# Kernel tuning notes

Hardware: AMD Instinct MI355X
Metric: run time of the kernel (lower is better)

## Reference

```python
import jax, jax.numpy as jnp
import numpy as np

ALPHA = 0.01  # ELU slope from init kwargs


def setup_inputs() -> dict:
    key = jax.random.key(0)
    k1, k2, k3, k4, k5 = jax.random.split(key, 5)
    B, L, D_IN, D_ATT = 8, 2048, 256, 128
    context = jax.random.normal(k1, (B, L, D_IN), dtype=jnp.float32)
    query = jax.random.normal(k2, (B, L, D_IN), dtype=jnp.float32)
    query_mask = jax.random.randint(k3, (B, L), 0, 2, dtype=jnp.int32)
    # Linear(in_size, attention_size, bias=False) weights (stored as [in, out])
    W_in = jax.random.normal(k4, (D_IN, D_ATT), dtype=jnp.float32) * 0.05
    W_mem = jax.random.normal(k5, (D_IN, D_ATT), dtype=jnp.float32) * 0.05
    return {"context": context, "query": query, "W_in": W_in,
            "W_mem": W_mem, "query_mask": query_mask}


def reference(context, query, W_in, W_mem, query_mask):
    # VariationalDropout is identity at inference; Linear -> ELU(alpha=0.01)
    inp = jax.nn.elu(jnp.einsum('bld,df->blf', context, W_in), ALPHA)   # [B, Lc, Datt]
    mem = jax.nn.elu(jnp.einsum('bld,df->blf', query, W_mem), ALPHA)    # [B, Lq, Datt]
    scale = inp.shape[-1] ** 0.5
    logits = jnp.einsum('bcf,bqf->bcq', inp, mem) / scale               # [B, Lc, Lq]
    big = jnp.finfo(logits.dtype).max
    # mask_diag=True: kill diagonal (self) positions
    Lq = logits.shape[-1]
    eye = jnp.eye(Lq, dtype=bool)
    logits = jnp.where(eye[None, :, :], -big, logits)
    # masked_softmax over the query axis using query_mask [B, Lq]
    valid = (query_mask > 0)[:, None, :]                                # [B, 1, Lq]
    logits = jnp.where(valid, logits, -big)
    score = jax.nn.softmax(logits, axis=-1)                             # [B, Lc, Lq]
    return jnp.einsum('bcq,bqd->bcd', score, query)                     # [B, Lc, D_in]
```

## Files before the change

### kernel.cpp

```cpp
#include <hip/hip_runtime.h>
#include <math.h>

typedef short v4s __attribute__((ext_vector_type(4)));
typedef short v8s __attribute__((ext_vector_type(8)));
typedef float v4f __attribute__((ext_vector_type(4)));

#define L2E 1.4426950408889634f
#define INV_SCALE 0.08838834764831845f
#define SCL2 (INV_SCALE * L2E)

static __device__ __forceinline__ short f2bf(float x) {
    union { float f; unsigned u; } c; c.f = x;
    unsigned u = c.u;
    unsigned r = (u + 0x7fffu + ((u >> 16) & 1u)) >> 16;
    return (short)r;
}

typedef __attribute__((address_space(3))) void lds_vt;
typedef __attribute__((address_space(1))) const void gl_vt;
static __device__ __forceinline__ void gload_lds16(const void* g, void* l) {
    __builtin_amdgcn_global_load_lds((gl_vt*)g, (lds_vt*)l, 16, 0, 0);
}

__global__ __launch_bounds__(256) void k_pre(const float* __restrict__ ctx,
                                             const float* __restrict__ qry,
                                             const float* __restrict__ Win,
                                             const float* __restrict__ Wmem,
                                             const int* __restrict__ qmask,
                                             short* __restrict__ Qa,
                                             short* __restrict__ Ka,
                                             short* __restrict__ VaT,
                                             float* __restrict__ maskadd) {
    __shared__ __align__(16) short WtS[128 * 132];
    __shared__ __align__(16) short Tt[256 * 72];
    int x = blockIdx.x;
    int tid = threadIdx.x;
    int msel = x & 255, isel = x >> 8;
    const float* X = isel ? qry : ctx;
    const float* W = isel ? Wmem : Win;
    short* Y = isel ? Ka : Qa;

    int w = tid >> 6, lane = tid & 63;
    int ln = lane & 15, qd = lane >> 4;
    int m0 = msel * 64 + w * 16;
    v4f zero = {0.f, 0.f, 0.f, 0.f};
    v4f o[8];
#pragma unroll
    for (int i = 0; i < 8; ++i) o[i] = zero;

#pragma unroll 1
    for (int kh = 0; kh < 2; ++kh) {
        if (kh) __syncthreads();
#pragma unroll 8
        for (int i = 0; i < 64; ++i) {
            int id = i * 256 + tid;
            int k = id >> 7, fp = id & 127;
            WtS[fp * 132 + k] = f2bf(W[(kh * 128 + k) * 128 + fp]);
        }
        __syncthreads();
#pragma unroll
        for (int kk = 0; kk < 4; ++kk) {
            const float* xp = X + (size_t)(m0 + ln) * 256 + kh * 128 + kk * 32 + qd * 8;
            float4 x0 = *(const float4*)xp;
            float4 x1 = *(const float4*)(xp + 4);
            v8s a;
            a[0] = f2bf(x0.x); a[1] = f2bf(x0.y); a[2] = f2bf(x0.z); a[3] = f2bf(x0.w);
            a[4] = f2bf(x1.x); a[5] = f2bf(x1.y); a[6] = f2bf(x1.z); a[7] = f2bf(x1.w);
            if (isel) {
#pragma unroll
                for (int si = 0; si < 8; ++si)
                    Tt[(kh * 128 + kk * 32 + qd * 8 + si) * 72 + (w * 16 + ln)] = a[si];
            }
#pragma unroll
            for (int nt = 0; nt < 8; ++nt) {
                v8s bfr = *(const v8s*)(WtS + (nt * 16 + ln) * 132 + kk * 32 + qd * 8);
                o[nt] = __builtin_amdgcn_mfma_f32_16x16x32_bf16(a, bfr, o[nt], 0, 0, 0);
            }
        }
    }
#pragma unroll
    for (int nt = 0; nt < 8; ++nt) {
#pragma unroll
        for (int r = 0; r < 4; ++r) {
            float v = o[nt][r];
            v = v > 0.f ? v : 0.01f * (__expf(v) - 1.f);
            Y[(size_t)(m0 + qd * 4 + r) * 128 + nt * 16 + ln] = f2bf(v);
        }
    }

    if (isel) {
        __syncthreads();
        int b2 = msel >> 5, q0 = (msel & 31) * 64;
        int dr = tid >> 3, j = tid & 7;
#pragma unroll
        for (int i = 0; i < 8; ++i) {
            int d = dr + i * 32;
            v8s vv = *(const v8s*)(Tt + d * 72 + j * 8);
            *(v8s*)(VaT + ((size_t)(b2 * 256 + d)) * 2048 + q0 + ((j ^ (d & 7)) << 3)) = vv;
        }
        if (tid < 64) {
            int qq = b2 * 2048 + q0 + tid;
            maskadd[qq] = (qmask[qq] > 0) ? 0.f : -__builtin_inff();
        }
    }
}

__global__ __launch_bounds__(512, 2) void k_attn(const short* __restrict__ Qa,
                                                 const short* __restrict__ Ka,
                                                 const short* __restrict__ VaT,
                                                 const float* __restrict__ maskadd,
                                                 float* __restrict__ out) {
    __shared__ __align__(16) short VaS[2][2][256 * 64];
    __shared__ __align__(16) short PS[2][64 * 64];
    __shared__ float lS[8 * 64];

    const int STEPS = 16;
    int blk = blockIdx.x;
    int b = blk & 7;
    int c0 = (blk >> 3) * 64;

    int tid = threadIdx.x;
    int w = tid >> 6, lane = tid & 63, ln = lane & 15, qd = lane >> 4;
    int g = w >> 2, wl = w & 3;
    int kv0 = g * 1024;

    const short* qbase = Qa + (size_t)(b * 2048) * 128;
    const short* kbase = Ka + (size_t)(b * 2048 + kv0 + wl * 16 + ln) * 128 + qd * 8;
    const short* vbase = VaT + (size_t)(b * 256) * 2048;
    const float* mbase = maskadd + b * 2048 + kv0 + wl * 16 + qd * 4;

    v8s qf[4][4];
#pragma unroll
    for (int ct = 0; ct < 4; ++ct) {
        const short* qp = qbase + (size_t)(c0 + ct * 16 + ln) * 128 + qd * 8;
#pragma unroll
        for (int kk = 0; kk < 4; ++kk) qf[ct][kk] = *(const v8s*)(qp + kk * 32);
    }

    v4f zero = {0.f, 0.f, 0.f, 0.f};
    v4f o[4][4];
#pragma unroll
    for (int i = 0; i < 4; ++i)
#pragma unroll
        for (int j = 0; j < 4; ++j) o[i][j] = zero;
    float lacc[4] = {0.f, 0.f, 0.f, 0.f};

    auto stageV = [&](int q0s, int buf) {
        short* base = &VaS[g][buf][0] + wl * 4096;
#pragma unroll
        for (int j = 0; j < 8; ++j) {
            int U = (wl * 8 + j) * 64 + lane;
            int d = U >> 3, cc = U & 7;
            gload_lds16(vbase + (size_t)d * 2048 + q0s + cc * 8,
                        base + j * 512);
        }
    };

    v8s kfA[4], kfB[4];
    float4 mkA, mkB;
    stageV(kv0, 0);
    asm volatile("" ::: "memory");
#pragma unroll
    for (int kk = 0; kk < 4; ++kk) kfA[kk] = *(const v8s*)(kbase + kk * 32);
    mkA = *(const float4*)(mbase);
    asm volatile("" ::: "memory");
    stageV(kv0 + 64, 1);

#define ATT_STEP(IT, KFC, MKC, KFN, MKN) do {                                  \
    int q0 = kv0 + (IT) * 64;                                                  \
    int itn = ((IT) + 1) & (STEPS - 1);                                        \
    int itn2 = ((IT) + 2) & (STEPS - 1);                                       \
    {              \
        const short* kp = kbase + (size_t)itn * 8192;                          \
        _Pragma("unroll")                                                      \
        for (int kk = 0; kk < 4; ++kk) KFN[kk] = *(const v8s*)(kp + kk * 32);  \
        MKN = *(const float4*)(mbase + itn * 64);                              \
    }                                                                          \
        \
    asm volatile("s_waitcnt vmcnt(13)" ::: "memory");                          \
    int kvb = q0 + wl * 16 + qd * 4;                                           \
    _Pragma("unroll")                                                          \
    for (int ct = 0; ct < 4; ++ct) {                                           \
        v4f s = zero;                                                          \
        _Pragma("unroll")                                                      \
        for (int kk = 0; kk < 4; ++kk)                                         \
            s = __builtin_amdgcn_mfma_f32_16x16x32_bf16(KFC[kk], qf[ct][kk],   \
                                                        s, 0, 0, 0);           \
        int cg = c0 + ct * 16 + ln;                                            \
        v4s pw;                                                                \
        float ls = 0.f;                                                        \
        _Pragma("unroll")                                                      \
        for (int r = 0; r < 4; ++r) {                                          \
            float v = s[r] * SCL2 + (&MKC.x)[r];                               \
            if (kvb + r == cg) v = -__builtin_inff();                          \
            float p = exp2f(v);                                                \
            ls += p;                                                           \
            pw[r] = f2bf(p);                                                   \
        }                                                                      \
        lacc[ct] += ls;                                                        \
        int hs = ((wl * 2 + (qd >> 1)) ^ (ln & 7));                            \
        *(v4s*)(&PS[g][0] + (ct * 16 + ln) * 64 + hs * 8 + (qd & 1) * 4) = pw; \
    }                                                                          \
    asm volatile("s_waitcnt lgkmcnt(0)" ::: "memory");                         \
    __builtin_amdgcn_s_barrier();                               \
    const short* vs = &VaS[g][(IT) & 1][0];                                    \
    __builtin_amdgcn_s_setprio(1);                                             \
    _Pragma("unroll")                                                          \
    for (int kk2 = 0; kk2 < 2; ++kk2) {                                        \
        v8s pf[4], vf[4];                                                      \
        _Pragma("unroll")                                                      \
        for (int ct = 0; ct < 4; ++ct)                                         \
            pf[ct] = *(const v8s*)(&PS[g][0] + (ct * 16 + ln) * 64 +           \
                                   (((kk2 * 4 + qd) ^ (ln & 7)) << 3));        \
        _Pragma("unroll")                                                      \
        for (int dt = 0; dt < 4; ++dt) {                                       \
            int d = wl * 64 + dt * 16 + ln;                                    \
            vf[dt] = *(const v8s*)(vs + d * 64 +                               \
                                   (((kk2 * 4 + qd) ^ (ln & 7)) << 3));        \
        }                                                                      \
        _Pragma("unroll")                                                      \
        for (int ct = 0; ct < 4; ++ct)                                         \
            _Pragma("unroll")                                                  \
            for (int dt = 0; dt < 4; ++dt)                                     \
                o[ct][dt] = __builtin_amdgcn_mfma_f32_16x16x32_bf16(           \
                    pf[ct], vf[dt], o[ct][dt], 0, 0, 0);                       \
    }                                                                          \
    __builtin_amdgcn_s_setprio(0);                                             \
            \
    asm volatile("s_waitcnt lgkmcnt(0)" ::: "memory");                         \
    stageV(kv0 + itn2 * 64, (IT) & 1);                                         \
    __builtin_amdgcn_s_barrier();                \
} while (0)

#pragma unroll 1
    for (int it2 = 0; it2 < STEPS; it2 += 2) {
        ATT_STEP(it2, kfA, mkA, kfB, mkB);
        ATT_STEP(it2 + 1, kfB, mkB, kfA, mkA);
    }
#undef ATT_STEP

    asm volatile("s_waitcnt vmcnt(0)" ::: "memory");
    __syncthreads();

#pragma unroll
    for (int ct = 0; ct < 4; ++ct) {
        float v = lacc[ct];
        v += __shfl_xor(v, 16);
        v += __shfl_xor(v, 32);
        if (qd == 0) lS[w * 64 + ct * 16 + ln] = v;
    }

    float* OS = (float*)&VaS[0][0][0];
    if (g == 1) {
#pragma unroll
        for (int ct = 0; ct < 4; ++ct)
#pragma unroll
            for (int r = 0; r < 4; ++r)
#pragma unroll
                for (int dt = 0; dt < 4; ++dt)
                    OS[(ct * 16 + qd * 4 + r) * 260 + wl * 64 + dt * 16 + ln] =
                        o[ct][dt][r];
    }
    __syncthreads();

    if (g == 0) {
#pragma unroll
        for (int ct = 0; ct < 4; ++ct) {
            float lv[4];
#pragma unroll
            for (int r = 0; r < 4; ++r) {
                float s = 0.f;
#pragma unroll
                for (int wv = 0; wv < 8; ++wv)
                    s += lS[wv * 64 + ct * 16 + qd * 4 + r];
                lv[r] = s;
            }
            int rowg = b * 2048 + c0 + ct * 16 + qd * 4;
#pragma unroll
            for (int r = 0; r < 4; ++r) {
                float inv = 1.f / lv[r];
#pragma unroll
                for (int dt = 0; dt < 4; ++dt) {
                    int col = wl * 64 + dt * 16 + ln;
                    float sum = o[ct][dt][r] +
                                OS[(ct * 16 + qd * 4 + r) * 260 + col];
                    out[(size_t)(rowg + r) * 256 + col] = sum * inv;
                }
            }
        }
    }
}

extern "C" void kernel_launch(void* const* d_in, const int* in_sizes, int n_in,
                              void* d_out, int out_size, void* d_ws, size_t ws_size,
                              hipStream_t stream) {
    const float* ctx  = (const float*)d_in[0];
    const float* qry  = (const float*)d_in[1];
    const float* win  = (const float*)d_in[2];
    const float* wmem = (const float*)d_in[3];
    const int* qmask  = (const int*)d_in[4];
    float* out = (float*)d_out;

    char* ws = (char*)d_ws;
    short* Qa      = (short*)(ws);
    short* Ka      = (short*)(ws + (4u << 20));
    short* VaT     = (short*)(ws + (8u << 20));
    float* maskadd = (float*)(ws + (16u << 20));

    k_pre<<<dim3(512), 256, 0, stream>>>(ctx, qry, win, wmem, qmask,
                                         Qa, Ka, VaT, maskadd);
    k_attn<<<dim3(256), 512, 0, stream>>>(Qa, Ka, VaT, maskadd, out);
}
```

Before: 144.8 us.

## Load V fragments directly from global and double-buffer P to halve LDS

Drops the asynchronous global-to-LDS staging of the transposed V tiles. Each wave now loads its V MFMA operands straight from global memory into registers every step, using the swizzle that the pre-pass already wrote. The P tile becomes double-buffered, so the trailing barrier in each step can go. Shared memory falls from about 149KB to about 70KB, which should let two 512-thread blocks share a CU. The cost is that V load latency is no longer prefetched two steps ahead and is only partly hidden by the softmax work.

After: 148.5 us. 1.03x slower.

```diff
diff --git a/kernel.cpp b/kernel.cpp
--- a/kernel.cpp
+++ b/kernel.cpp
@@ -14,12 +14,6 @@
     unsigned u = c.u;
     unsigned r = (u + 0x7fffu + ((u >> 16) & 1u)) >> 16;
     return (short)r;
-}
-
-typedef __attribute__((address_space(3))) void lds_vt;
-typedef __attribute__((address_space(1))) const void gl_vt;
-static __device__ __forceinline__ void gload_lds16(const void* g, void* l) {
-    __builtin_amdgcn_global_load_lds((gl_vt*)g, (lds_vt*)l, 16, 0, 0);
 }
 
 __global__ __launch_bounds__(256) void k_pre(const float* __restrict__ ctx,
@@ -110,9 +104,10 @@
                                                  const short* __restrict__ VaT,
                                                  const float* __restrict__ maskadd,
                                                  float* __restrict__ out) {
-    __shared__ __align__(16) short VaS[2][2][256 * 64];
-    __shared__ __align__(16) short PS[2][64 * 64];
-    __shared__ float lS[8 * 64];
+    __shared__ __align__(16) char smem[70272];
+    short* PSbase = (short*)smem;
+    float* OS = (float*)smem;
+    float* lS = (float*)(smem + 68224);
 
     const int STEPS = 16;
     int blk = blockIdx.x;
@@ -123,6 +118,7 @@
     int w = tid >> 6, lane = tid & 63, ln = lane & 15, qd = lane >> 4;
     int g = w >> 2, wl = w & 3;
     int kv0 = g * 1024;
+    short* PSg = PSbase + g * 16384;
 
     const short* qbase = Qa + (size_t)(b * 2048) * 128;
     const short* kbase = Ka + (size_t)(b * 2048 + kv0 + wl * 16 + ln) * 128 + qd * 8;
@@ -145,39 +141,22 @@
         for (int j = 0; j < 4; ++j) o[i][j] = zero;
     float lacc[4] = {0.f, 0.f, 0.f, 0.f};
 
-    auto stageV = [&](int q0s, int buf) {
-        short* base = &VaS[g][buf][0] + wl * 4096;
-#pragma unroll
-        for (int j = 0; j < 8; ++j) {
-            int U = (wl * 8 + j) * 64 + lane;
-            int d = U >> 3, cc = U & 7;
-            gload_lds16(vbase + (size_t)d * 2048 + q0s + cc * 8,
-                        base + j * 512);
-        }
-    };
-
     v8s kfA[4], kfB[4];
     float4 mkA, mkB;
-    stageV(kv0, 0);
-    asm volatile("" ::: "memory");
 #pragma unroll
     for (int kk = 0; kk < 4; ++kk) kfA[kk] = *(const v8s*)(kbase + kk * 32);
     mkA = *(const float4*)(mbase);
-    asm volatile("" ::: "memory");
-    stageV(kv0 + 64, 1);
 
 #define ATT_STEP(IT, KFC, MKC, KFN, MKN) do {                                  \
     int q0 = kv0 + (IT) * 64;                                                  \
     int itn = ((IT) + 1) & (STEPS - 1);                                        \
-    int itn2 = ((IT) + 2) & (STEPS - 1);                                       \
     {              \
         const short* kp = kbase + (size_t)itn * 8192;                          \
         _Pragma("unroll")                                                      \
         for (int kk = 0; kk < 4; ++kk) KFN[kk] = *(const v8s*)(kp + kk * 32);  \
         MKN = *(const float4*)(mbase + itn * 64);                              \
     }                                                                          \
-        \
-    asm volatile("s_waitcnt vmcnt(13)" ::: "memory");                          \
+    short* PSc = PSg + ((IT) & 1) * 8192;                                      \
     int kvb = q0 + wl * 16 + qd * 4;                                           \
     _Pragma("unroll")                                                          \
     for (int ct = 0; ct < 4; ++ct) {                                           \
@@ -199,37 +178,39 @@
         }                                                                      \
         lacc[ct] += ls;                                                        \
         int hs = ((wl * 2 + (qd >> 1)) ^ (ln & 7));                            \
-        *(v4s*)(&PS[g][0] + (ct * 16 + ln) * 64 + hs * 8 + (qd & 1) * 4) = pw; \
+        *(v4s*)(PSc + (ct * 16 + ln) * 64 + hs * 8 + (qd & 1) * 4) = pw;       \
+    }                                                                          \
+           \
+    v8s vf2[2][4];                                                             \
+    {                                                                          \
+        const short* vp = vbase + q0;                                          \
+        _Pragma("unroll")                                                      \
+        for (int kk2 = 0; kk2 < 2; ++kk2) {                                    \
+            int xg = ((kk2 * 4 + qd) ^ (ln & 7)) << 3;                         \
+            _Pragma("unroll")                                                  \
+            for (int dt = 0; dt < 4; ++dt)                                     \
+                vf2[kk2][dt] = *(const v8s*)(vp +                              \
+                    (size_t)(wl * 64 + dt * 16 + ln) * 2048 + xg);             \
+        }                                                                      \
     }                                                                          \
     asm volatile("s_waitcnt lgkmcnt(0)" ::: "memory");                         \
-    __builtin_amdgcn_s_barrier();                               \
-    const short* vs = &VaS[g][(IT) & 1][0];                                    \
+    __builtin_amdgcn_s_barrier();             \
     __builtin_amdgcn_s_setprio(1);                                             \
     _Pragma("unroll")                                                          \
     for (int kk2 = 0; kk2 < 2; ++kk2) {                                        \
-        v8s pf[4], vf[4];                                                      \
+        v8s pf[4];                                                             \
         _Pragma("unroll")                                                      \
         for (int ct = 0; ct < 4; ++ct)                                         \
-            pf[ct] = *(const v8s*)(&PS[g][0] + (ct * 16 + ln) * 64 +           \
+            pf[ct] = *(const v8s*)(PSc + (ct * 16 + ln) * 64 +                 \
                                    (((kk2 * 4 + qd) ^ (ln & 7)) << 3));        \
-        _Pragma("unroll")                                                      \
-        for (int dt = 0; dt < 4; ++dt) {                                       \
-            int d = wl * 64 + dt * 16 + ln;                                    \
-            vf[dt] = *(const v8s*)(vs + d * 64 +                               \
-                                   (((kk2 * 4 + qd) ^ (ln & 7)) << 3));        \
-        }                                                                      \
         _Pragma("unroll")                                                      \
         for (int ct = 0; ct < 4; ++ct)                                         \
             _Pragma("unroll")                                                  \
             for (int dt = 0; dt < 4; ++dt)                                     \
                 o[ct][dt] = __builtin_amdgcn_mfma_f32_16x16x32_bf16(           \
-                    pf[ct], vf[dt], o[ct][dt], 0, 0, 0);                       \
+                    pf[ct], vf2[kk2][dt], o[ct][dt], 0, 0, 0);                 \
     }                                                                          \
     __builtin_amdgcn_s_setprio(0);                                             \
-            \
-    asm volatile("s_waitcnt lgkmcnt(0)" ::: "memory");                         \
-    stageV(kv0 + itn2 * 64, (IT) & 1);                                         \
-    __builtin_amdgcn_s_barrier();                \
 } while (0)
 
 #pragma unroll 1
@@ -239,7 +220,6 @@
     }
 #undef ATT_STEP
 
-    asm volatile("s_waitcnt vmcnt(0)" ::: "memory");
     __syncthreads();
 
 #pragma unroll
@@ -250,7 +230,6 @@
         if (qd == 0) lS[w * 64 + ct * 16 + ln] = v;
     }
 
-    float* OS = (float*)&VaS[0][0][0];
     if (g == 1) {
 #pragma unroll
         for (int ct = 0; ct < 4; ++ct)
```
